# Kernel tuning notes

Hardware: AMD Instinct MI355X
Metric: run time of the kernel (lower is better)

Reference implementation:

```python
import jax, jax.numpy as jnp
import numpy as np


def setup_inputs() -> dict:
    key = jax.random.key(0)
    x = jax.random.normal(key, (64, 512, 16, 16), dtype=jnp.float32)
    return {"x": x}


def reference(x):
    # x: [B, dim, h, w] -> covariance pooling y: [B, dim, dim]
    B, dim, h, w = x.shape
    M = h * w
    xf = x.reshape(B, dim, M)
    # I_hat = (1/M) I - (1/M^2) 11^T  (centering matrix scaled by 1/M)
    inv_M = jnp.asarray(1.0 / M, dtype=x.dtype)
    I_hat = inv_M * jnp.eye(M, dtype=x.dtype) - (inv_M * inv_M) * jnp.ones((M, M), dtype=x.dtype)
    # y = x @ I_hat @ x^T, I_hat broadcast over batch
    xI = jnp.einsum('bdm,mn->bdn', xf, I_hat)   # [B, dim, M]
    y = jnp.einsum('bdn,ben->bde', xI, xf)      # [B, dim, dim]
    return y
```

## Files before the change

### kernel.cpp

```cpp
#include <hip/hip_runtime.h>
#include <hip/hip_bf16.h>
#include <stdint.h>


typedef __attribute__((ext_vector_type(8))) short bf16x8;
typedef __attribute__((ext_vector_type(4))) float f32x4;

static __device__ __forceinline__ unsigned short f2bf(float f) {
    union { float f; uint32_t u; } c; c.f = f;
    uint32_t u = c.u;
    return (unsigned short)((u + 0x7FFFu + ((u >> 16) & 1u)) >> 16);
}

__global__ __launch_bounds__(256) void center_bf16(const float* __restrict__ x,
                                                   unsigned short* __restrict__ xb) {
    const int wave = threadIdx.x >> 6;
    const int lane = threadIdx.x & 63;
    const int row  = blockIdx.x * 4 + wave;
    const f32x4 v = __builtin_nontemporal_load(((const f32x4*)(x + (size_t)row * 256)) + lane);
    float s = v.x + v.y + v.z + v.w;
#pragma unroll
    for (int off = 32; off > 0; off >>= 1)
        s += __shfl_xor(s, off, 64);
    const float mean = s * (1.0f / 256.0f);
    const float sc = 0.0625f;
    ushort4 o;
    o.x = f2bf((v.x - mean) * sc);
    o.y = f2bf((v.y - mean) * sc);
    o.z = f2bf((v.z - mean) * sc);
    o.w = f2bf((v.w - mean) * sc);
    ((ushort4*)(xb + (size_t)row * 256))[lane] = o;
}

static __device__ __forceinline__ void gl_lds16(const unsigned short* g, unsigned short* l) {
    __builtin_amdgcn_global_load_lds(
        (const __attribute__((address_space(1))) unsigned int*)g,
        (__attribute__((address_space(3))) unsigned int*)l,
        16, 0, 0);
}

__global__ __launch_bounds__(256) void syrk_bf16(const unsigned short* __restrict__ xb,
                                                 float* __restrict__ y) {
    __shared__ unsigned short As[128 * 32];
    __shared__ unsigned short Bs[128 * 32];

    const int xcd  = blockIdx.x & 7;
    const int j    = blockIdx.x >> 3;
    const int b    = xcd * 8 + (j >> 4);
    const int tile = j & 15;
    const int tm = tile >> 2, tn = tile & 3;

    const unsigned short* Abase = xb + ((size_t)b * 512 + tm * 128) * 256;
    const unsigned short* Bbase = xb + ((size_t)b * 512 + tn * 128) * 256;

    const int tid  = threadIdx.x;
    const int lane = tid & 63;
    const int wave = tid >> 6;
    const int wm = (wave >> 1) * 64;
    const int wn = (wave & 1) * 64;

    f32x4 acc[4][4] = {};

    const int rl = lane & 15;
    const int swl = ((lane >> 4) ^ ((rl >> 1) & 3)) * 8;

    for (int kk = 0; kk < 256; kk += 32) {
        __syncthreads();
#pragma unroll
        for (int t = 0; t < 2; ++t) {
            const int e   = t * 256 + tid;
            const int row = e >> 2;
            const int g   = ((e & 3) ^ ((e >> 3) & 3)) * 8;
            gl_lds16(Abase + row * 256 + kk + g, As + e * 8);
            gl_lds16(Bbase + row * 256 + kk + g, Bs + e * 8);
        }
        __syncthreads();

        bf16x8 af[4], bfr[4];
#pragma unroll
        for (int i = 0; i < 4; ++i)
            af[i] = *(const bf16x8*)(As + (wm + i * 16 + rl) * 32 + swl);
#pragma unroll
        for (int jj = 0; jj < 4; ++jj)
            bfr[jj] = *(const bf16x8*)(Bs + (wn + jj * 16 + rl) * 32 + swl);
#pragma unroll
        for (int i = 0; i < 4; ++i)
#pragma unroll
            for (int jj = 0; jj < 4; ++jj)
                acc[i][jj] = __builtin_amdgcn_mfma_f32_16x16x32_bf16(
                    af[i], bfr[jj], acc[i][jj], 0, 0, 0);
    }

    float* ybase = y + (size_t)b * 512 * 512;
    const int rowb = tm * 128 + wm + (lane >> 4) * 4;
    const int colb = tn * 128 + wn + (lane & 15);
#pragma unroll
    for (int i = 0; i < 4; ++i) {
#pragma unroll
        for (int jj = 0; jj < 4; ++jj) {
            const int col = colb + jj * 16;
            const int r0  = rowb + i * 16;
#pragma unroll
            for (int r = 0; r < 4; ++r)
                __builtin_nontemporal_store(acc[i][jj][r],
                    ybase + (size_t)(r0 + r) * 512 + col);
        }
    }
}

extern "C" void kernel_launch(void* const* d_in, const int* in_sizes, int n_in,
                              void* d_out, int out_size, void* d_ws, size_t ws_size,
                              hipStream_t stream) {
    const float* x = (const float*)d_in[0];
    float* yout = (float*)d_out;
    unsigned short* xb = (unsigned short*)d_ws;

    center_bf16<<<8192, 256, 0, stream>>>(x, xb);
    syrk_bf16<<<1024, 256, 0, stream>>>(xb, yout);
}
```

Before: 111.4 us.

## Fuse centering into SYRK via rank-1 mean correction and diagonal tile reuse

Drops the separate centering kernel and the bf16 workspace round trip. The GEMM now loads fp32 x directly, scales it, converts it to bf16 into LDS and accumulates row sums. The mean is removed afterwards with a rank-1 correction (y = x·xᵀ − μ_a·μ_bᵀ). Diagonal tiles load only the A tile and reuse it as B. The tradeoffs are that each block now reads fp32 (twice the bytes) through register-staged loads instead of async global-to-LDS, and that uncentered bf16 products followed by subtraction can lose accuracy.

```diff
diff --git a/kernel.cpp b/kernel.cpp
--- a/kernel.cpp
+++ b/kernel.cpp
@@ -1,5 +1,4 @@
 #include <hip/hip_runtime.h>
-#include <hip/hip_bf16.h>
 #include <stdint.h>
 
 
@@ -12,46 +11,22 @@
     return (unsigned short)((u + 0x7FFFu + ((u >> 16) & 1u)) >> 16);
 }
 
-__global__ __launch_bounds__(256) void center_bf16(const float* __restrict__ x,
-                                                   unsigned short* __restrict__ xb) {
-    const int wave = threadIdx.x >> 6;
-    const int lane = threadIdx.x & 63;
-    const int row  = blockIdx.x * 4 + wave;
-    const f32x4 v = __builtin_nontemporal_load(((const f32x4*)(x + (size_t)row * 256)) + lane);
-    float s = v.x + v.y + v.z + v.w;
-#pragma unroll
-    for (int off = 32; off > 0; off >>= 1)
-        s += __shfl_xor(s, off, 64);
-    const float mean = s * (1.0f / 256.0f);
-    const float sc = 0.0625f;
-    ushort4 o;
-    o.x = f2bf((v.x - mean) * sc);
-    o.y = f2bf((v.y - mean) * sc);
-    o.z = f2bf((v.z - mean) * sc);
-    o.w = f2bf((v.w - mean) * sc);
-    ((ushort4*)(xb + (size_t)row * 256))[lane] = o;
-}
-
-static __device__ __forceinline__ void gl_lds16(const unsigned short* g, unsigned short* l) {
-    __builtin_amdgcn_global_load_lds(
-        (const __attribute__((address_space(1))) unsigned int*)g,
-        (__attribute__((address_space(3))) unsigned int*)l,
-        16, 0, 0);
-}
-
-__global__ __launch_bounds__(256) void syrk_bf16(const unsigned short* __restrict__ xb,
-                                                 float* __restrict__ y) {
-    __shared__ unsigned short As[128 * 32];
-    __shared__ unsigned short Bs[128 * 32];
+__global__ __launch_bounds__(256) void covpool_fused(const float* __restrict__ x,
+                                                     float* __restrict__ y) {
+    __shared__ __align__(16) unsigned short As[128 * 32];
+    __shared__ __align__(16) unsigned short Bs[128 * 32];
+    __shared__ __align__(16) float muA[128];
+    __shared__ __align__(16) float muB[128];
 
     const int xcd  = blockIdx.x & 7;
     const int j    = blockIdx.x >> 3;
     const int b    = xcd * 8 + (j >> 4);
     const int tile = j & 15;
     const int tm = tile >> 2, tn = tile & 3;
+    const bool diag = (tm == tn);
 
-    const unsigned short* Abase = xb + ((size_t)b * 512 + tm * 128) * 256;
-    const unsigned short* Bbase = xb + ((size_t)b * 512 + tn * 128) * 256;
+    const float* Ag = x + ((size_t)b * 512 + tm * 128) * 256;
+    const float* Bg = x + ((size_t)b * 512 + tn * 128) * 256;
 
     const int tid  = threadIdx.x;
     const int lane = tid & 63;
@@ -60,29 +35,56 @@
     const int wn = (wave & 1) * 64;
 
     f32x4 acc[4][4] = {};
+    float pA[2] = {0.f, 0.f}, pB[2] = {0.f, 0.f};
 
-    const int rl = lane & 15;
+    const int rl  = lane & 15;
     const int swl = ((lane >> 4) ^ ((rl >> 1) & 3)) * 8;
+    const int srow   = tid >> 2;
+    const int schunk = tid & 3;
 
     for (int kk = 0; kk < 256; kk += 32) {
         __syncthreads();
 #pragma unroll
         for (int t = 0; t < 2; ++t) {
-            const int e   = t * 256 + tid;
-            const int row = e >> 2;
-            const int g   = ((e & 3) ^ ((e >> 3) & 3)) * 8;
-            gl_lds16(Abase + row * 256 + kk + g, As + e * 8);
-            gl_lds16(Bbase + row * 256 + kk + g, Bs + e * 8);
+            const int row  = t * 64 + srow;
+            const int slot = schunk ^ ((row >> 1) & 3);
+            {
+                const float* g = Ag + (size_t)row * 256 + kk + schunk * 8;
+                f32x4 v0 = *(const f32x4*)g;
+                f32x4 v1 = *(const f32x4*)(g + 4);
+                v0 *= 0.0625f; v1 *= 0.0625f;
+                pA[t] += (v0.x + v0.y + v0.z + v0.w) + (v1.x + v1.y + v1.z + v1.w);
+                bf16x8 o;
+                o[0] = (short)f2bf(v0.x); o[1] = (short)f2bf(v0.y);
+                o[2] = (short)f2bf(v0.z); o[3] = (short)f2bf(v0.w);
+                o[4] = (short)f2bf(v1.x); o[5] = (short)f2bf(v1.y);
+                o[6] = (short)f2bf(v1.z); o[7] = (short)f2bf(v1.w);
+                *(bf16x8*)(As + row * 32 + slot * 8) = o;
+            }
+            if (!diag) {
+                const float* g = Bg + (size_t)row * 256 + kk + schunk * 8;
+                f32x4 v0 = *(const f32x4*)g;
+                f32x4 v1 = *(const f32x4*)(g + 4);
+                v0 *= 0.0625f; v1 *= 0.0625f;
+                pB[t] += (v0.x + v0.y + v0.z + v0.w) + (v1.x + v1.y + v1.z + v1.w);
+                bf16x8 o;
+                o[0] = (short)f2bf(v0.x); o[1] = (short)f2bf(v0.y);
+                o[2] = (short)f2bf(v0.z); o[3] = (short)f2bf(v0.w);
+                o[4] = (short)f2bf(v1.x); o[5] = (short)f2bf(v1.y);
+                o[6] = (short)f2bf(v1.z); o[7] = (short)f2bf(v1.w);
+                *(bf16x8*)(Bs + row * 32 + slot * 8) = o;
+            }
         }
         __syncthreads();
 
+        const unsigned short* Bsrc = diag ? As : Bs;
         bf16x8 af[4], bfr[4];
 #pragma unroll
         for (int i = 0; i < 4; ++i)
             af[i] = *(const bf16x8*)(As + (wm + i * 16 + rl) * 32 + swl);
 #pragma unroll
         for (int jj = 0; jj < 4; ++jj)
-            bfr[jj] = *(const bf16x8*)(Bs + (wn + jj * 16 + rl) * 32 + swl);
+            bfr[jj] = *(const bf16x8*)(Bsrc + (wn + jj * 16 + rl) * 32 + swl);
 #pragma unroll
         for (int i = 0; i < 4; ++i)
 #pragma unroll
@@ -91,19 +93,36 @@
                     af[i], bfr[jj], acc[i][jj], 0, 0, 0);
     }
 
+#pragma unroll
+    for (int t = 0; t < 2; ++t) {
+        float s = pA[t];
+        s += __shfl_xor(s, 1, 64); s += __shfl_xor(s, 2, 64);
+        if ((tid & 3) == 0) muA[t * 64 + srow] = s * 0.0625f;
+        if (!diag) {
+            float sb = pB[t];
+            sb += __shfl_xor(sb, 1, 64); sb += __shfl_xor(sb, 2, 64);
+            if ((tid & 3) == 0) muB[t * 64 + srow] = sb * 0.0625f;
+        }
+    }
+    __syncthreads();
+
+    const float* muBp = diag ? muA : muB;
     float* ybase = y + (size_t)b * 512 * 512;
     const int rowb = tm * 128 + wm + (lane >> 4) * 4;
-    const int colb = tn * 128 + wn + (lane & 15);
+    const int colb = tn * 128 + wn + rl;
+    float cB[4];
+#pragma unroll
+    for (int jj = 0; jj < 4; ++jj) cB[jj] = muBp[wn + jj * 16 + rl];
 #pragma unroll
     for (int i = 0; i < 4; ++i) {
+        const f32x4 ma = *(const f32x4*)&muA[wm + i * 16 + (lane >> 4) * 4];
 #pragma unroll
         for (int jj = 0; jj < 4; ++jj) {
             const int col = colb + jj * 16;
             const int r0  = rowb + i * 16;
 #pragma unroll
             for (int r = 0; r < 4; ++r)
-                __builtin_nontemporal_store(acc[i][jj][r],
-                    ybase + (size_t)(r0 + r) * 512 + col);
+                ybase[(size_t)(r0 + r) * 512 + col] = acc[i][jj][r] - ma[r] * cB[jj];
         }
     }
 }
@@ -113,8 +132,6 @@
                               hipStream_t stream) {
     const float* x = (const float*)d_in[0];
     float* yout = (float*)d_out;
-    unsigned short* xb = (unsigned short*)d_ws;
-
-    center_bf16<<<8192, 256, 0, stream>>>(x, xb);
-    syrk_bf16<<<1024, 256, 0, stream>>>(xb, yout);
+    (void)d_ws; (void)ws_size;
+    covpool_fused<<<1024, 256, 0, stream>>>(x, yout);
 }
```

Measured after the change: 110.5 us. About the same (-0.8%).
